# Kernel optimization log

Hardware: AMD Instinct MI355X
Metric: run time of the kernel (lower is better)

Reference implementation:

```python
import jax, jax.numpy as jnp
import numpy as np

THRESH = 1.0
GAMA = 1.0
TAU0 = 0.5

# ZIF surrogate spike: forward hard step, backward triangular surrogate
@jax.custom_vjp
def zif(x):
    return (x > 0).astype(x.dtype)

def _zif_fwd(x):
    return zif(x), x

def _zif_bwd(x, g):
    surr = (1.0 / GAMA) * (1.0 / GAMA) * jnp.clip(GAMA - jnp.abs(x), 0.0, None)
    return (g * surr,)

zif.defvjp(_zif_fwd, _zif_bwd)


def setup_inputs() -> dict:
    key = jax.random.key(0)
    k1, k2, k3, k4, k5 = jax.random.split(key, 5)
    B, T, C, H, W = 32, 8, 128, 32, 32
    red = 4
    x = jax.random.normal(k1, (B, T, C, H, W), dtype=jnp.float32)
    # fc1: Linear(C, C//red); fc2: Linear(C//red, 1); PyTorch default init scale
    s1 = 1.0 / np.sqrt(C)
    s2 = 1.0 / np.sqrt(C // red)
    w1 = jax.random.uniform(k2, (C // red, C), jnp.float32, -s1, s1)
    b1 = jax.random.uniform(k3, (C // red,), jnp.float32, -s1, s1)
    w2 = jax.random.uniform(k4, (1, C // red), jnp.float32, -s2, s2)
    b2 = jax.random.uniform(k5, (1,), jnp.float32, -s2, s2)
    return {"x": x, "w1": w1, "b1": b1, "w2": w2, "b2": b2}


def reference(x, w1, b1, w2, b2):
    B, T, C, H, W = x.shape

    def step(carry, xt):
        mem, tau = carry  # mem: [B,C,H,W], tau: [B,1,1,1]
        mem = mem * tau + xt
        # SE-style gating MLP on channel means
        x_mean = jnp.mean(mem, axis=(-1, -2))          # [B,C]
        embed = jax.nn.relu(x_mean @ w1.T + b1)        # [B,C//r]
        lifp = jax.nn.sigmoid(embed @ w2.T + b2)       # [B,1]
        new_tau = lifp[:, :, None, None]               # [B,1,1,1]
        spike = zif(mem - THRESH)
        mem = (1.0 - spike) * mem
        return (mem, new_tau), spike

    mem0 = jnp.zeros((B, C, H, W), dtype=x.dtype)
    tau0 = jnp.full((B, 1, 1, 1), TAU0, dtype=x.dtype)
    xt = jnp.transpose(x, (1, 0, 2, 3, 4))  # [T,B,C,H,W]
    _, spikes = jax.lax.scan(step, (mem0, tau0), xt)
    return jnp.transpose(spikes, (1, 0, 2, 3, 4))  # [B,T,C,H,W]
```

## Files before the change

### kernel.cpp

```cpp
#include <hip/hip_runtime.h>

typedef float v4f __attribute__((ext_vector_type(4)));

#define NB   32
#define NT   8
#define NC   128
#define NQ   256
#define CRED 32
#define PADI 32

__device__ int                g_arrive[NB * PADI];
__device__ unsigned long long g_xsum[2 * NB * NC];

__global__ __launch_bounds__(256)
void lif_init() {
    int i = threadIdx.x + blockIdx.x * blockDim.x;
    if (i < NB * PADI) g_arrive[i] = 0;
}

__global__ __launch_bounds__(256, 4)
void dynamic_lif(const float* __restrict__ x,
                 const float* __restrict__ w1,
                 const float* __restrict__ b1,
                 const float* __restrict__ w2,
                 const float* __restrict__ b2,
                 float* __restrict__ out)
{
    const int bid = blockIdx.x;
    const int b   = bid >> 5;
    const int c0  = (bid & 31) << 2;
    const int tid = threadIdx.x;
    const int wv  = tid >> 6;
    const int ln  = tid & 63;

    __shared__ double s_part[4][4];
    __shared__ float  s_tau;

    const v4f* __restrict__ x4 = (const v4f*)x;
    v4f* __restrict__ o4       = (v4f*)out;

    v4f mem[4];
    #pragma unroll
    for (int p = 0; p < 4; ++p) mem[p] = (v4f){0.f, 0.f, 0.f, 0.f};

    float tau = 0.5f;

    v4f xv[4];
    #pragma unroll
    for (int p = 0; p < 4; ++p)
        xv[p] = __builtin_nontemporal_load(x4 + ((b * NT + 0) * NC + c0 + p) * NQ + tid);

    for (int t = 0; t < NT; ++t) {
        double psum[4];
        #pragma unroll
        for (int p = 0; p < 4; ++p) {
            v4f m = mem[p];
            m.x = fmaf(m.x, tau, xv[p].x);
            m.y = fmaf(m.y, tau, xv[p].y);
            m.z = fmaf(m.z, tau, xv[p].z);
            m.w = fmaf(m.w, tau, xv[p].w);
            psum[p] = ((double)m.x + (double)m.y) + ((double)m.z + (double)m.w);
            v4f sp;
            sp.x = (m.x > 1.0f) ? 1.0f : 0.0f;
            sp.y = (m.y > 1.0f) ? 1.0f : 0.0f;
            sp.z = (m.z > 1.0f) ? 1.0f : 0.0f;
            sp.w = (m.w > 1.0f) ? 1.0f : 0.0f;
            __builtin_nontemporal_store(sp, o4 + ((b * NT + t) * NC + c0 + p) * NQ + tid);
            m.x = (m.x > 1.0f) ? 0.0f : m.x;
            m.y = (m.y > 1.0f) ? 0.0f : m.y;
            m.z = (m.z > 1.0f) ? 0.0f : m.z;
            m.w = (m.w > 1.0f) ? 0.0f : m.w;
            mem[p] = m;
        }

        if (t + 1 < NT) {
            #pragma unroll
            for (int p = 0; p < 4; ++p)
                xv[p] = __builtin_nontemporal_load(
                    x4 + ((b * NT + (t + 1)) * NC + c0 + p) * NQ + tid);
        }

        #pragma unroll
        for (int p = 0; p < 4; ++p) {
            double s = psum[p];
            #pragma unroll
            for (int off = 32; off > 0; off >>= 1) s += __shfl_down(s, off);
            if (ln == 0) s_part[p][wv] = s;
        }
        __syncthreads();
        if (tid < 4) {
            double s = (s_part[tid][0] + s_part[tid][1]) +
                       (s_part[tid][2] + s_part[tid][3]);
            double mean = s * (1.0 / 1024.0);
            unsigned long long bits = __double_as_longlong(mean);
            __hip_atomic_store(&g_xsum[(t & 1) * (NB * NC) + b * NC + c0 + tid],
                               bits, __ATOMIC_RELAXED, __HIP_MEMORY_SCOPE_AGENT);
        }
        __syncthreads();

        if (t == NT - 1) break;

        if (tid == 0) {
            __hip_atomic_fetch_add(&g_arrive[b * PADI], 1,
                                   __ATOMIC_RELAXED, __HIP_MEMORY_SCOPE_AGENT);
            const int target = 32 * (t + 1);
            while (__hip_atomic_load(&g_arrive[b * PADI],
                                     __ATOMIC_RELAXED, __HIP_MEMORY_SCOPE_AGENT) < target)
                __builtin_amdgcn_s_sleep(2);
        }
        __syncthreads();

        double e = 0.0;
        if (tid < CRED) {
            const unsigned long long* __restrict__ xm =
                g_xsum + (t & 1) * (NB * NC) + b * NC;
            const float* __restrict__ w1r = w1 + tid * NC;
            double acc = (double)b1[tid];
            #pragma unroll 8
            for (int cc = 0; cc < NC; ++cc) {
                unsigned long long mb =
                    __hip_atomic_load(&xm[cc], __ATOMIC_RELAXED,
                                      __HIP_MEMORY_SCOPE_AGENT);
                acc += __longlong_as_double(mb) * (double)w1r[cc];
            }
            double emb = acc > 0.0 ? acc : 0.0;
            e = emb * (double)w2[tid];
        }
        #pragma unroll
        for (int off = 32; off > 0; off >>= 1) e += __shfl_down(e, off);
        if (tid == 0) {
            double z = e + (double)b2[0];
            s_tau = (float)(1.0 / (1.0 + exp(-z)));
        }
        __syncthreads();
        tau = s_tau;
    }
}

extern "C" void kernel_launch(void* const* d_in, const int* in_sizes, int n_in,
                              void* d_out, int out_size, void* d_ws, size_t ws_size,
                              hipStream_t stream) {
    const float* x  = (const float*)d_in[0];
    const float* w1 = (const float*)d_in[1];
    const float* b1 = (const float*)d_in[2];
    const float* w2 = (const float*)d_in[3];
    const float* b2 = (const float*)d_in[4];
    float* out      = (float*)d_out;

    hipLaunchKernelGGL(lif_init, dim3((NB * PADI + 255) / 256), dim3(256),
                       0, stream);
    hipLaunchKernelGGL(dynamic_lif, dim3(NB * NC / 4), dim3(256), 0, stream,
                       x, w1, b1, w2, b2, out);
}
```

Before: 296.9 us.

## Make each wavefront own one channel and sync per-wave without block barriers

Each wavefront now processes a whole channel (1024 elements), so the channel mean needs only an intra-wave shuffle reduction instead of an LDS plus __syncthreads reduction. Every wave publishes its mean and arrives on the global per-batch counter itself, then spins independently, which removes all block-level barriers. The gating MLP is split across all 64 lanes of each wave, with the two halves of the dot product combined by a shuffle, rather than run serially by 32 threads. The next timestep's loads are issued before the spin-wait. The cost is 4x more atomic arrivals and spinning waves per batch, and every wave redundantly computes the MLP.

```diff
diff --git a/kernel.cpp b/kernel.cpp
--- a/kernel.cpp
+++ b/kernel.cpp
@@ -26,114 +26,110 @@
                  const float* __restrict__ b2,
                  float* __restrict__ out)
 {
-    const int bid = blockIdx.x;
-    const int b   = bid >> 5;
-    const int c0  = (bid & 31) << 2;
     const int tid = threadIdx.x;
+    const int ln  = tid & 63;
     const int wv  = tid >> 6;
-    const int ln  = tid & 63;
+    const int gw  = blockIdx.x * 4 + wv;
+    const int b   = gw >> 7;
+    const int c   = gw & 127;
 
-    __shared__ double s_part[4][4];
-    __shared__ float  s_tau;
+    __shared__ double s_mlp[4][NC];
 
     const v4f* __restrict__ x4 = (const v4f*)x;
     v4f* __restrict__ o4       = (v4f*)out;
 
     v4f mem[4];
     #pragma unroll
-    for (int p = 0; p < 4; ++p) mem[p] = (v4f){0.f, 0.f, 0.f, 0.f};
+    for (int q = 0; q < 4; ++q) mem[q] = (v4f){0.f, 0.f, 0.f, 0.f};
 
     float tau = 0.5f;
 
     v4f xv[4];
-    #pragma unroll
-    for (int p = 0; p < 4; ++p)
-        xv[p] = __builtin_nontemporal_load(x4 + ((b * NT + 0) * NC + c0 + p) * NQ + tid);
+    {
+        const long base0 = ((long)(b * NT + 0) * NC + c) * NQ;
+        #pragma unroll
+        for (int q = 0; q < 4; ++q)
+            xv[q] = __builtin_nontemporal_load(x4 + base0 + ln + 64 * q);
+    }
 
     for (int t = 0; t < NT; ++t) {
-        double psum[4];
+        const long obase = ((long)(b * NT + t) * NC + c) * NQ;
+        double ps = 0.0;
         #pragma unroll
-        for (int p = 0; p < 4; ++p) {
-            v4f m = mem[p];
-            m.x = fmaf(m.x, tau, xv[p].x);
-            m.y = fmaf(m.y, tau, xv[p].y);
-            m.z = fmaf(m.z, tau, xv[p].z);
-            m.w = fmaf(m.w, tau, xv[p].w);
-            psum[p] = ((double)m.x + (double)m.y) + ((double)m.z + (double)m.w);
+        for (int q = 0; q < 4; ++q) {
+            v4f m = mem[q];
+            m.x = fmaf(m.x, tau, xv[q].x);
+            m.y = fmaf(m.y, tau, xv[q].y);
+            m.z = fmaf(m.z, tau, xv[q].z);
+            m.w = fmaf(m.w, tau, xv[q].w);
+            ps += ((double)m.x + (double)m.y) + ((double)m.z + (double)m.w);
             v4f sp;
             sp.x = (m.x > 1.0f) ? 1.0f : 0.0f;
             sp.y = (m.y > 1.0f) ? 1.0f : 0.0f;
             sp.z = (m.z > 1.0f) ? 1.0f : 0.0f;
             sp.w = (m.w > 1.0f) ? 1.0f : 0.0f;
-            __builtin_nontemporal_store(sp, o4 + ((b * NT + t) * NC + c0 + p) * NQ + tid);
+            __builtin_nontemporal_store(sp, o4 + obase + ln + 64 * q);
             m.x = (m.x > 1.0f) ? 0.0f : m.x;
             m.y = (m.y > 1.0f) ? 0.0f : m.y;
             m.z = (m.z > 1.0f) ? 0.0f : m.z;
             m.w = (m.w > 1.0f) ? 0.0f : m.w;
-            mem[p] = m;
+            mem[q] = m;
         }
-
-        if (t + 1 < NT) {
-            #pragma unroll
-            for (int p = 0; p < 4; ++p)
-                xv[p] = __builtin_nontemporal_load(
-                    x4 + ((b * NT + (t + 1)) * NC + c0 + p) * NQ + tid);
-        }
-
-        #pragma unroll
-        for (int p = 0; p < 4; ++p) {
-            double s = psum[p];
-            #pragma unroll
-            for (int off = 32; off > 0; off >>= 1) s += __shfl_down(s, off);
-            if (ln == 0) s_part[p][wv] = s;
-        }
-        __syncthreads();
-        if (tid < 4) {
-            double s = (s_part[tid][0] + s_part[tid][1]) +
-                       (s_part[tid][2] + s_part[tid][3]);
-            double mean = s * (1.0 / 1024.0);
-            unsigned long long bits = __double_as_longlong(mean);
-            __hip_atomic_store(&g_xsum[(t & 1) * (NB * NC) + b * NC + c0 + tid],
-                               bits, __ATOMIC_RELAXED, __HIP_MEMORY_SCOPE_AGENT);
-        }
-        __syncthreads();
 
         if (t == NT - 1) break;
 
-        if (tid == 0) {
+        #pragma unroll
+        for (int off = 32; off > 0; off >>= 1) ps += __shfl_down(ps, off);
+
+        if (ln == 0)
+            __hip_atomic_store(&g_xsum[(t & 1) * (NB * NC) + b * NC + c],
+                               __double_as_longlong(ps * (1.0 / 1024.0)),
+                               __ATOMIC_RELAXED, __HIP_MEMORY_SCOPE_AGENT);
+        __builtin_amdgcn_s_waitcnt(0);
+        if (ln == 0)
             __hip_atomic_fetch_add(&g_arrive[b * PADI], 1,
                                    __ATOMIC_RELAXED, __HIP_MEMORY_SCOPE_AGENT);
-            const int target = 32 * (t + 1);
-            while (__hip_atomic_load(&g_arrive[b * PADI],
-                                     __ATOMIC_RELAXED, __HIP_MEMORY_SCOPE_AGENT) < target)
-                __builtin_amdgcn_s_sleep(2);
+
+        {
+            const long basen = ((long)(b * NT + (t + 1)) * NC + c) * NQ;
+            #pragma unroll
+            for (int q = 0; q < 4; ++q)
+                xv[q] = __builtin_nontemporal_load(x4 + basen + ln + 64 * q);
         }
-        __syncthreads();
 
+        const int target = 128 * (t + 1);
+        while (__hip_atomic_load(&g_arrive[b * PADI],
+                                 __ATOMIC_RELAXED, __HIP_MEMORY_SCOPE_AGENT) < target)
+            __builtin_amdgcn_s_sleep(2);
+
+        {
+            const unsigned long long* __restrict__ xmb =
+                g_xsum + (t & 1) * (NB * NC) + b * NC;
+            unsigned long long u0 =
+                __hip_atomic_load(&xmb[ln], __ATOMIC_RELAXED, __HIP_MEMORY_SCOPE_AGENT);
+            unsigned long long u1 =
+                __hip_atomic_load(&xmb[ln + 64], __ATOMIC_RELAXED, __HIP_MEMORY_SCOPE_AGENT);
+            s_mlp[wv][ln]      = __longlong_as_double(u0);
+            s_mlp[wv][ln + 64] = __longlong_as_double(u1);
+        }
+        const int h = ln & 31, half = ln >> 5;
+        const float*  __restrict__ w1r = w1 + h * NC + half * 64;
+        const double* __restrict__ xr  = &s_mlp[wv][half * 64];
+        double acc = 0.0;
+        #pragma unroll
+        for (int j = 0; j < 64; ++j) acc += xr[j] * (double)w1r[j];
+        acc += __shfl_down(acc, 32);
         double e = 0.0;
-        if (tid < CRED) {
-            const unsigned long long* __restrict__ xm =
-                g_xsum + (t & 1) * (NB * NC) + b * NC;
-            const float* __restrict__ w1r = w1 + tid * NC;
-            double acc = (double)b1[tid];
-            #pragma unroll 8
-            for (int cc = 0; cc < NC; ++cc) {
-                unsigned long long mb =
-                    __hip_atomic_load(&xm[cc], __ATOMIC_RELAXED,
-                                      __HIP_MEMORY_SCOPE_AGENT);
-                acc += __longlong_as_double(mb) * (double)w1r[cc];
-            }
-            double emb = acc > 0.0 ? acc : 0.0;
-            e = emb * (double)w2[tid];
+        if (ln < CRED) {
+            double full = acc + (double)b1[ln];
+            double emb  = full > 0.0 ? full : 0.0;
+            e = emb * (double)w2[ln];
         }
         #pragma unroll
-        for (int off = 32; off > 0; off >>= 1) e += __shfl_down(e, off);
-        if (tid == 0) {
-            double z = e + (double)b2[0];
-            s_tau = (float)(1.0 / (1.0 + exp(-z)));
-        }
-        __syncthreads();
-        tau = s_tau;
+        for (int off = 16; off > 0; off >>= 1) e += __shfl_down(e, off);
+        double z = e + (double)b2[0];
+        float ntau = (float)(1.0 / (1.0 + exp(-z)));
+        tau = __shfl(ntau, 0);
     }
 }
 
```

After: 497.4 us. 1.68x slower.

## Split LIF into tau-computation pass and separate spike-writing pass

Applied to the files above, without the earlier changes.

The fused kernel becomes two kernels. The first runs the recurrent mean and MLP gating with grid-wide per-batch barriers, computes only the tau values for each timestep and stores them globally, and no longer writes output or reads the last timestep. A second, fully parallel kernel rereads x, recomputes membrane dynamics using the stored taus, and writes spikes. This takes output stores off the barrier-synchronised critical path and switches loads to normal cached accesses. The cost is reading x twice, about 7/8 extra, plus one more kernel launch.

```diff
diff --git a/kernel.cpp b/kernel.cpp
--- a/kernel.cpp
+++ b/kernel.cpp
@@ -11,6 +11,7 @@
 
 __device__ int                g_arrive[NB * PADI];
 __device__ unsigned long long g_xsum[2 * NB * NC];
+__device__ float              g_tau[NB * NT];
 
 __global__ __launch_bounds__(256)
 void lif_init() {
@@ -19,12 +20,11 @@
 }
 
 __global__ __launch_bounds__(256, 4)
-void dynamic_lif(const float* __restrict__ x,
-                 const float* __restrict__ w1,
-                 const float* __restrict__ b1,
-                 const float* __restrict__ w2,
-                 const float* __restrict__ b2,
-                 float* __restrict__ out)
+void lif_tau(const float* __restrict__ x,
+             const float* __restrict__ w1,
+             const float* __restrict__ b1,
+             const float* __restrict__ w2,
+             const float* __restrict__ b2)
 {
     const int bid = blockIdx.x;
     const int b   = bid >> 5;
@@ -37,7 +37,6 @@
     __shared__ float  s_tau;
 
     const v4f* __restrict__ x4 = (const v4f*)x;
-    v4f* __restrict__ o4       = (v4f*)out;
 
     v4f mem[4];
     #pragma unroll
@@ -48,9 +47,9 @@
     v4f xv[4];
     #pragma unroll
     for (int p = 0; p < 4; ++p)
-        xv[p] = __builtin_nontemporal_load(x4 + ((b * NT + 0) * NC + c0 + p) * NQ + tid);
+        xv[p] = x4[((b * NT + 0) * NC + c0 + p) * NQ + tid];
 
-    for (int t = 0; t < NT; ++t) {
+    for (int t = 0; t < NT - 1; ++t) {
         double psum[4];
         #pragma unroll
         for (int p = 0; p < 4; ++p) {
@@ -60,12 +59,6 @@
             m.z = fmaf(m.z, tau, xv[p].z);
             m.w = fmaf(m.w, tau, xv[p].w);
             psum[p] = ((double)m.x + (double)m.y) + ((double)m.z + (double)m.w);
-            v4f sp;
-            sp.x = (m.x > 1.0f) ? 1.0f : 0.0f;
-            sp.y = (m.y > 1.0f) ? 1.0f : 0.0f;
-            sp.z = (m.z > 1.0f) ? 1.0f : 0.0f;
-            sp.w = (m.w > 1.0f) ? 1.0f : 0.0f;
-            __builtin_nontemporal_store(sp, o4 + ((b * NT + t) * NC + c0 + p) * NQ + tid);
             m.x = (m.x > 1.0f) ? 0.0f : m.x;
             m.y = (m.y > 1.0f) ? 0.0f : m.y;
             m.z = (m.z > 1.0f) ? 0.0f : m.z;
@@ -73,11 +66,10 @@
             mem[p] = m;
         }
 
-        if (t + 1 < NT) {
+        if (t + 1 < NT - 1) {
             #pragma unroll
             for (int p = 0; p < 4; ++p)
-                xv[p] = __builtin_nontemporal_load(
-                    x4 + ((b * NT + (t + 1)) * NC + c0 + p) * NQ + tid);
+                xv[p] = x4[((b * NT + (t + 1)) * NC + c0 + p) * NQ + tid];
         }
 
         #pragma unroll
@@ -91,14 +83,11 @@
         if (tid < 4) {
             double s = (s_part[tid][0] + s_part[tid][1]) +
                        (s_part[tid][2] + s_part[tid][3]);
-            double mean = s * (1.0 / 1024.0);
-            unsigned long long bits = __double_as_longlong(mean);
             __hip_atomic_store(&g_xsum[(t & 1) * (NB * NC) + b * NC + c0 + tid],
-                               bits, __ATOMIC_RELAXED, __HIP_MEMORY_SCOPE_AGENT);
+                               __double_as_longlong(s * (1.0 / 1024.0)),
+                               __ATOMIC_RELAXED, __HIP_MEMORY_SCOPE_AGENT);
         }
         __syncthreads();
-
-        if (t == NT - 1) break;
 
         if (tid == 0) {
             __hip_atomic_fetch_add(&g_arrive[b * PADI], 1,
@@ -130,10 +119,51 @@
         for (int off = 32; off > 0; off >>= 1) e += __shfl_down(e, off);
         if (tid == 0) {
             double z = e + (double)b2[0];
-            s_tau = (float)(1.0 / (1.0 + exp(-z)));
+            float nt_tau = (float)(1.0 / (1.0 + exp(-z)));
+            s_tau = nt_tau;
+            if ((bid & 31) == 0)
+                g_tau[b * NT + t + 1] = nt_tau;
         }
         __syncthreads();
         tau = s_tau;
+    }
+}
+
+__global__ __launch_bounds__(256)
+void lif_spike(const float* __restrict__ x, float* __restrict__ out)
+{
+    const int bid = blockIdx.x;
+    const int b   = bid >> 7;
+    const int c   = bid & 127;
+    const int tid = threadIdx.x;
+
+    const v4f* __restrict__ x4 = (const v4f*)x;
+    v4f* __restrict__ o4       = (v4f*)out;
+
+    float taus[NT];
+    taus[0] = 0.5f;
+    #pragma unroll
+    for (int t = 1; t < NT; ++t) taus[t] = g_tau[b * NT + t];
+
+    v4f m = (v4f){0.f, 0.f, 0.f, 0.f};
+    #pragma unroll
+    for (int t = 0; t < NT; ++t) {
+        const long idx = ((long)(b * NT + t) * NC + c) * NQ + tid;
+        v4f xv = x4[idx];
+        m.x = fmaf(m.x, taus[t], xv.x);
+        m.y = fmaf(m.y, taus[t], xv.y);
+        m.z = fmaf(m.z, taus[t], xv.z);
+        m.w = fmaf(m.w, taus[t], xv.w);
+        v4f sp;
+        sp.x = (m.x > 1.0f) ? 1.0f : 0.0f;
+        sp.y = (m.y > 1.0f) ? 1.0f : 0.0f;
+        sp.z = (m.z > 1.0f) ? 1.0f : 0.0f;
+        sp.w = (m.w > 1.0f) ? 1.0f : 0.0f;
+        __builtin_nontemporal_store(sp, o4 + idx);
+        m.x = (m.x > 1.0f) ? 0.0f : m.x;
+        m.y = (m.y > 1.0f) ? 0.0f : m.y;
+        m.z = (m.z > 1.0f) ? 0.0f : m.z;
+        m.w = (m.w > 1.0f) ? 0.0f : m.w;
     }
 }
 
@@ -149,6 +179,8 @@
 
     hipLaunchKernelGGL(lif_init, dim3((NB * PADI + 255) / 256), dim3(256),
                        0, stream);
-    hipLaunchKernelGGL(dynamic_lif, dim3(NB * NC / 4), dim3(256), 0, stream,
-                       x, w1, b1, w2, b2, out);
+    hipLaunchKernelGGL(lif_tau, dim3(NB * NC / 4), dim3(256), 0, stream,
+                       x, w1, b1, w2, b2);
+    hipLaunchKernelGGL(lif_spike, dim3(NB * NC), dim3(256), 0, stream,
+                       x, out);
 }
```

Result: slower. 388.5 us (+30.8%).
